# Kernel tuning notes

Measured on AMD Instinct MI355X. Metric: run time of the kernel, lower is better.

## Reference

```python
import jax, jax.numpy as jnp
import numpy as np

IN_SHAPE = (8, 16, 8)     # hidden_shape, prod = 1024
FF_SHAPE = (16, 16, 16)   # ff_shape, prod = 4096
RANKS = (1, 8, 8, 1)      # tt_ranks


def _make_cores(key, in_shape, out_shape, ranks):
    cores = []
    for k in range(3):
        key, sub = jax.random.split(key)
        shape = (ranks[k], in_shape[k], out_shape[k], ranks[k + 1])
        # glorot-ish scale per core
        scale = (2.0 / (in_shape[k] * ranks[k] + out_shape[k] * ranks[k + 1])) ** 0.5
        cores.append(jax.random.normal(sub, shape, dtype=jnp.float32) * scale)
    return key, cores


def setup_inputs() -> dict:
    key = jax.random.key(0)
    key, kx = jax.random.split(key)
    x = jax.random.normal(kx, (8192, int(np.prod(IN_SHAPE))), dtype=jnp.float32)
    key, c0 = _make_cores(key, IN_SHAPE, FF_SHAPE, RANKS)
    key, c1 = _make_cores(key, FF_SHAPE, IN_SHAPE, RANKS)
    b0 = jnp.zeros((int(np.prod(FF_SHAPE)),), dtype=jnp.float32)
    b1 = jnp.zeros((int(np.prod(IN_SHAPE)),), dtype=jnp.float32)
    return {
        "x": x,
        "c0a": c0[0], "c0b": c0[1], "c0c": c0[2], "b0": b0,
        "c1a": c1[0], "c1b": c1[1], "c1c": c1[2], "b1": b1,
    }


def tt_linear(x, cores, bias, in_shape, out_shape):
    # x: (B, prod(in_shape)); cores[k]: (r_k, in_k, out_k, r_{k+1})
    B = x.shape[0]
    t = x.reshape(B, *in_shape)                      # (B, i, j, k)
    t = jnp.einsum('bijk,aior->bjkor', t, cores[0])  # (B, j, k, o1, r1)
    t = jnp.einsum('bjkor,rjps->bkops', t, cores[1]) # (B, k, o1, o2, r2)
    t = jnp.einsum('bkops,skqu->bopq', t, cores[2])  # (B, o1, o2, o3)
    return t.reshape(B, -1) + bias


def reference(x, c0a, c0b, c0c, b0, c1a, c1b, c1c, b1):
    h = tt_linear(x, (c0a, c0b, c0c), b0, IN_SHAPE, FF_SHAPE)
    h = jax.nn.gelu(h, approximate=False)  # nn.GELU default = exact erf form
    out = tt_linear(h, (c1a, c1b, c1c), b1, FF_SHAPE, IN_SHAPE)
    return out
```

## Files before the change

### kernel.cpp

```cpp
#include <hip/hip_runtime.h>
#include <math.h>

typedef _Float16 f16x8 __attribute__((ext_vector_type(8)));
typedef _Float16 f16x4 __attribute__((ext_vector_type(4)));
typedef float f32x16 __attribute__((ext_vector_type(16)));

__device__ __forceinline__ void async_copy16(const void* g, void* l) {
    __builtin_amdgcn_global_load_lds(
        (const __attribute__((address_space(1))) void*)g,
        (__attribute__((address_space(3))) void*)l, 16, 0, 0);
}

__global__ __launch_bounds__(256) void prep_kernel(
    const float* __restrict__ x, _Float16* __restrict__ xh,
    const float* __restrict__ c0a, const float* __restrict__ c0b,
    const float* __restrict__ c0c, _Float16* __restrict__ W0t,
    const float* __restrict__ c1a, const float* __restrict__ c1b,
    const float* __restrict__ c1c, _Float16* __restrict__ W1t) {
    __shared__ float G[16384];
    const int b = blockIdx.x, t = threadIdx.x;
    if (b < 1024) {
        const float4* in4 = (const float4*)x;
        f16x4* out4 = (f16x4*)xh;
        const int base = b * 2048 + t;
#pragma unroll
        for (int u = 0; u < 8; ++u) {
            float4 v = in4[base + u * 256];
            f16x4 o;
            o[0] = (_Float16)v.x; o[1] = (_Float16)v.y;
            o[2] = (_Float16)v.z; o[3] = (_Float16)v.w;
            out4[base + u * 256] = o;
        }
    } else if (b < 1280) {
        const int o = (b - 1024) >> 4, p = (b - 1024) & 15;
        {
            const int h = t >> 7, qk = t & 127, q = qk >> 3, k = qk & 7;
            float cr[8];
#pragma unroll
            for (int ss = 0; ss < 8; ++ss) cr[ss] = c0c[(ss * 8 + k) * 16 + q];
            for (int rj = h * 64; rj < h * 64 + 64; ++rj) {
                const float4* b4 = (const float4*)(c0b + (rj * 16 + p) * 8);
                float4 b0 = b4[0], b1 = b4[1];
                float s = b0.x * cr[0] + b0.y * cr[1] + b0.z * cr[2] + b0.w * cr[3]
                        + b1.x * cr[4] + b1.y * cr[5] + b1.z * cr[6] + b1.w * cr[7];
                G[q * 1024 + rj * 8 + k] = s;
            }
        }
        __syncthreads();
        const int i = t >> 5, j = (t >> 1) & 15, kq = t & 1;
        float a[8];
#pragma unroll
        for (int r = 0; r < 8; ++r) a[r] = c0a[(i * 16 + o) * 8 + r];
        const float4* G4 = (const float4*)G;
#pragma unroll
        for (int q = 0; q < 16; ++q) {
            float4 acc = {0.f, 0.f, 0.f, 0.f};
#pragma unroll
            for (int r = 0; r < 8; ++r) {
                float4 g = G4[q * 256 + r * 32 + j * 2 + kq];
                acc.x += a[r] * g.x; acc.y += a[r] * g.y;
                acc.z += a[r] * g.z; acc.w += a[r] * g.w;
            }
            f16x4 h4;
            h4[0] = (_Float16)acc.x; h4[1] = (_Float16)acc.y;
            h4[2] = (_Float16)acc.z; h4[3] = (_Float16)acc.w;
            *(f16x4*)(W0t + (size_t)((o * 16 + p) * 16 + q) * 1024 + t * 4) = h4;
        }
    } else {
        const int o = (b - 1280) >> 4, p = (b - 1280) & 15;
        {
            const int h = t >> 7, qk = t & 127, q = qk >> 4, k = qk & 15;
            float cr[8];
#pragma unroll
            for (int ss = 0; ss < 8; ++ss) cr[ss] = c1c[(ss * 16 + k) * 8 + q];
            for (int rj = h * 64; rj < h * 64 + 64; ++rj) {
                const float4* b4 = (const float4*)(c1b + (rj * 16 + p) * 8);
                float4 b0 = b4[0], b1 = b4[1];
                float s = b0.x * cr[0] + b0.y * cr[1] + b0.z * cr[2] + b0.w * cr[3]
                        + b1.x * cr[4] + b1.y * cr[5] + b1.z * cr[6] + b1.w * cr[7];
                G[q * 2048 + rj * 16 + k] = s;
            }
        }
        __syncthreads();
        const int ig = t >> 6, j = (t >> 2) & 15, kq = t & 3;
        float a[4][8];
#pragma unroll
        for (int ii = 0; ii < 4; ++ii)
#pragma unroll
            for (int r = 0; r < 8; ++r) a[ii][r] = c1a[((ig * 4 + ii) * 8 + o) * 8 + r];
        const float4* G4 = (const float4*)G;
#pragma unroll
        for (int q = 0; q < 8; ++q) {
            float4 acc[4] = {{0,0,0,0},{0,0,0,0},{0,0,0,0},{0,0,0,0}};
#pragma unroll
            for (int r = 0; r < 8; ++r) {
                float4 g = G4[q * 512 + r * 64 + j * 4 + kq];
#pragma unroll
                for (int ii = 0; ii < 4; ++ii) {
                    acc[ii].x += a[ii][r] * g.x; acc[ii].y += a[ii][r] * g.y;
                    acc[ii].z += a[ii][r] * g.z; acc[ii].w += a[ii][r] * g.w;
                }
            }
            const size_t rowbase = (size_t)((o * 16 + p) * 8 + q) * 4096;
#pragma unroll
            for (int ii = 0; ii < 4; ++ii) {
                f16x4 h4;
                h4[0] = (_Float16)acc[ii].x; h4[1] = (_Float16)acc[ii].y;
                h4[2] = (_Float16)acc[ii].z; h4[3] = (_Float16)acc[ii].w;
                *(f16x4*)(W1t + rowbase + (ig * 4 + ii) * 256 + j * 16 + kq * 4) = h4;
            }
        }
    }
}

template <int OUTMODE>
__global__ __launch_bounds__(256) void gemm32_kernel(
    const _Float16* __restrict__ A, const _Float16* __restrict__ Bt,
    const float* __restrict__ bias, void* __restrict__ Cout,
    int M, int N, int K) {
    constexpr int BK = 64;
    __shared__ alignas(16) _Float16 sA[128 * BK];
    __shared__ alignas(16) _Float16 sB[128 * BK];

    const int t = threadIdx.x, lane = t & 63, w = t >> 6;
    const int m0 = blockIdx.x * 128, n0 = blockIdx.y * 128;
    const int wm = (w & 1) * 64, wn = (w >> 1) * 64;
    const int l31 = lane & 31, lh = lane >> 5;

    f32x16 acc[2][2] = {};

    const int s0 = w * 256 + lane;
    const int row0 = s0 >> 3;
    const int cslot = s0 & 7;
    const int kofs = (cslot ^ (row0 & 7)) * 8;
    const _Float16* gA = A + (size_t)(m0 + row0) * K + kofs;
    const _Float16* gB = Bt + (size_t)(n0 + row0) * K + kofs;
    _Float16* lA = sA + s0 * 8;
    _Float16* lB = sB + s0 * 8;
    const size_t rs = (size_t)8 * K;

    for (int k0 = 0; k0 < K; k0 += BK) {
#pragma unroll
        for (int m = 0; m < 4; ++m) {
            async_copy16(gA + k0 + m * rs, lA + m * 512);
            async_copy16(gB + k0 + m * rs, lB + m * 512);
        }
        __syncthreads();
#pragma unroll
        for (int kk = 0; kk < 4; ++kk) {
            f16x8 af[2], bf[2];
            const int c = kk * 2 + lh;
            const int sl = (c ^ (l31 & 7)) * 8;
#pragma unroll
            for (int i = 0; i < 2; ++i) {
                af[i] = *(const f16x8*)(sA + (wm + i * 32 + l31) * BK + sl);
                bf[i] = *(const f16x8*)(sB + (wn + i * 32 + l31) * BK + sl);
            }
#pragma unroll
            for (int i = 0; i < 2; ++i)
#pragma unroll
                for (int j = 0; j < 2; ++j)
                    acc[i][j] = __builtin_amdgcn_mfma_f32_32x32x16_f16(af[i], bf[j], acc[i][j], 0, 0, 0);
        }
        __syncthreads();
    }

#pragma unroll
    for (int i = 0; i < 2; ++i)
#pragma unroll
        for (int j = 0; j < 2; ++j) {
            const int col = n0 + wn + j * 32 + l31;
            const float bv = bias[col];
            const int rbase = m0 + wm + i * 32 + 4 * lh;
            if (OUTMODE == 1) {
                _Float16* C = (_Float16*)Cout;
#pragma unroll
                for (int r = 0; r < 16; ++r) {
                    int row = rbase + (r & 3) + 8 * (r >> 2);
                    float v = acc[i][j][r] + bv;
                    float uu = v * (0.7978845608028654f + 0.0356774081363001f * v * v);
                    float e = __builtin_amdgcn_exp2f(uu * 2.8853900817779268f);
                    float rc = __builtin_amdgcn_rcpf(e + 1.0f);
                    C[(size_t)row * N + col] = (_Float16)(v * (1.0f - rc));
                }
            } else {
                float* C = (float*)Cout;
#pragma unroll
                for (int r = 0; r < 16; ++r) {
                    int row = rbase + (r & 3) + 8 * (r >> 2);
                    C[(size_t)row * N + col] = acc[i][j][r] + bv;
                }
            }
        }
}

__global__ __launch_bounds__(256) void gemm32_splitk(
    const _Float16* __restrict__ A, const _Float16* __restrict__ Bt,
    float* __restrict__ p0, float* __restrict__ p1,
    int M, int N, int K) {
    constexpr int BK = 64;
    __shared__ alignas(16) _Float16 sA[128 * BK];
    __shared__ alignas(16) _Float16 sB[128 * BK];

    const int t = threadIdx.x, lane = t & 63, w = t >> 6;
    const int m0 = blockIdx.x * 128, n0 = blockIdx.y * 128;
    const int wm = (w & 1) * 64, wn = (w >> 1) * 64;
    const int l31 = lane & 31, lh = lane >> 5;

    f32x16 acc[2][2] = {};

    const int s0 = w * 256 + lane;
    const int row0 = s0 >> 3;
    const int cslot = s0 & 7;
    const int kofs = (cslot ^ (row0 & 7)) * 8;
    const _Float16* gA = A + (size_t)(m0 + row0) * K + kofs;
    const _Float16* gB = Bt + (size_t)(n0 + row0) * K + kofs;
    _Float16* lA = sA + s0 * 8;
    _Float16* lB = sB + s0 * 8;
    const size_t rs = (size_t)8 * K;

    const int kbase = blockIdx.z * (K >> 1);
    const int kend = kbase + (K >> 1);
    for (int k0 = kbase; k0 < kend; k0 += BK) {
#pragma unroll
        for (int m = 0; m < 4; ++m) {
            async_copy16(gA + k0 + m * rs, lA + m * 512);
            async_copy16(gB + k0 + m * rs, lB + m * 512);
        }
        __syncthreads();
#pragma unroll
        for (int kk = 0; kk < 4; ++kk) {
            f16x8 af[2], bf[2];
            const int c = kk * 2 + lh;
            const int sl = (c ^ (l31 & 7)) * 8;
#pragma unroll
            for (int i = 0; i < 2; ++i) {
                af[i] = *(const f16x8*)(sA + (wm + i * 32 + l31) * BK + sl);
                bf[i] = *(const f16x8*)(sB + (wn + i * 32 + l31) * BK + sl);
            }
#pragma unroll
            for (int i = 0; i < 2; ++i)
#pragma unroll
                for (int j = 0; j < 2; ++j)
                    acc[i][j] = __builtin_amdgcn_mfma_f32_32x32x16_f16(af[i], bf[j], acc[i][j], 0, 0, 0);
        }
        __syncthreads();
    }

    float* C = blockIdx.z ? p1 : p0;
#pragma unroll
    for (int i = 0; i < 2; ++i)
#pragma unroll
        for (int j = 0; j < 2; ++j) {
            const int col = n0 + wn + j * 32 + l31;
            const int rbase = m0 + wm + i * 32 + 4 * lh;
#pragma unroll
            for (int r = 0; r < 16; ++r) {
                int row = rbase + (r & 3) + 8 * (r >> 2);
                C[(size_t)row * N + col] = acc[i][j][r];
            }
        }
}

__global__ __launch_bounds__(256) void reduce_bias(
    const float* __restrict__ p1, const float* __restrict__ bias,
    float* __restrict__ out, int total4, int N) {
    const float4* q4 = (const float4*)p1;
    float4* o4 = (float4*)out;
    for (int i = blockIdx.x * 256 + threadIdx.x; i < total4; i += gridDim.x * 256) {
        float4 o = o4[i], q = q4[i];
        const int col = (i << 2) & (N - 1);
        const float4 b = *(const float4*)(bias + col);
        o.x += q.x + b.x; o.y += q.y + b.y;
        o.z += q.z + b.z; o.w += q.w + b.w;
        o4[i] = o;
    }
}

extern "C" void kernel_launch(void* const* d_in, const int* in_sizes, int n_in,
                              void* d_out, int out_size, void* d_ws, size_t ws_size,
                              hipStream_t stream) {
    const float* x   = (const float*)d_in[0];
    const float* c0a = (const float*)d_in[1];
    const float* c0b = (const float*)d_in[2];
    const float* c0c = (const float*)d_in[3];
    const float* b0  = (const float*)d_in[4];
    const float* c1a = (const float*)d_in[5];
    const float* c1b = (const float*)d_in[6];
    const float* c1c = (const float*)d_in[7];
    const float* b1  = (const float*)d_in[8];
    float* out = (float*)d_out;

    char* ws = (char*)d_ws;
    _Float16* xh  = (_Float16*)(ws);
    _Float16* W0t = (_Float16*)(ws + (size_t)(16u << 20));
    _Float16* W1t = (_Float16*)(ws + (size_t)(24u << 20));
    _Float16* h   = (_Float16*)(ws + (size_t)(32u << 20));
    float*    p1  = (float*)   (ws + (size_t)(96u << 20));

    prep_kernel<<<dim3(1408), dim3(256), 0, stream>>>(
        x, xh, c0a, c0b, c0c, W0t, c1a, c1b, c1c, W1t);
    gemm32_kernel<1><<<dim3(64, 32), dim3(256), 0, stream>>>(
        xh, W0t, b0, (void*)h, 8192, 4096, 1024);
    if (ws_size >= ((size_t)128u << 20)) {
        gemm32_splitk<<<dim3(64, 8, 2), dim3(256), 0, stream>>>(
            h, W1t, out, p1, 8192, 1024, 4096);
        reduce_bias<<<dim3(2048), dim3(256), 0, stream>>>(
            p1, b1, out, (8192 * 1024) / 4, 1024);
    } else {
        gemm32_kernel<0><<<dim3(64, 8), dim3(256), 0, stream>>>(
            h, W1t, b1, (void*)out, 8192, 1024, 4096);
    }
}
```

Measured before the change: 283.2 us.

## Replace split-K partial buffer and reduce kernel with atomic adds; split prep blocks

The second GEMM's split-K halves now accumulate directly into the zeroed output with unsafe atomic float adds, with the bias added by the z=0 half. This removes the partial-sum buffer and the separate reduce kernel, at the cost of a memset of the output and atomic traffic. The weight-prep blocks are split in two over q, halving shared memory per block and doubling block count for more parallelism. The fallback path for small workspace is removed.

```diff
diff --git a/kernel.cpp b/kernel.cpp
--- a/kernel.cpp
+++ b/kernel.cpp
@@ -17,7 +17,7 @@
     const float* __restrict__ c0c, _Float16* __restrict__ W0t,
     const float* __restrict__ c1a, const float* __restrict__ c1b,
     const float* __restrict__ c1c, _Float16* __restrict__ W1t) {
-    __shared__ float G[16384];
+    __shared__ float G[8192];
     const int b = blockIdx.x, t = threadIdx.x;
     if (b < 1024) {
         const float4* in4 = (const float4*)x;
@@ -31,19 +31,21 @@
             o[2] = (_Float16)v.z; o[3] = (_Float16)v.w;
             out4[base + u * 256] = o;
         }
-    } else if (b < 1280) {
-        const int o = (b - 1024) >> 4, p = (b - 1024) & 15;
+    } else if (b < 1536) {
+        const int idx = b - 1024;
+        const int o = idx >> 5, p = (idx >> 1) & 15, qh = idx & 1;
         {
-            const int h = t >> 7, qk = t & 127, q = qk >> 3, k = qk & 7;
+            const int h = t >> 6, pair = t & 63, ql = pair >> 3, k = pair & 7;
+            const int q = qh * 8 + ql;
             float cr[8];
 #pragma unroll
             for (int ss = 0; ss < 8; ++ss) cr[ss] = c0c[(ss * 8 + k) * 16 + q];
-            for (int rj = h * 64; rj < h * 64 + 64; ++rj) {
+            for (int rj = h * 32; rj < h * 32 + 32; ++rj) {
                 const float4* b4 = (const float4*)(c0b + (rj * 16 + p) * 8);
                 float4 b0 = b4[0], b1 = b4[1];
                 float s = b0.x * cr[0] + b0.y * cr[1] + b0.z * cr[2] + b0.w * cr[3]
                         + b1.x * cr[4] + b1.y * cr[5] + b1.z * cr[6] + b1.w * cr[7];
-                G[q * 1024 + rj * 8 + k] = s;
+                G[ql * 1024 + rj * 8 + k] = s;
             }
         }
         __syncthreads();
@@ -53,11 +55,12 @@
         for (int r = 0; r < 8; ++r) a[r] = c0a[(i * 16 + o) * 8 + r];
         const float4* G4 = (const float4*)G;
 #pragma unroll
-        for (int q = 0; q < 16; ++q) {
+        for (int ql = 0; ql < 8; ++ql) {
+            const int q = qh * 8 + ql;
             float4 acc = {0.f, 0.f, 0.f, 0.f};
 #pragma unroll
             for (int r = 0; r < 8; ++r) {
-                float4 g = G4[q * 256 + r * 32 + j * 2 + kq];
+                float4 g = G4[ql * 256 + r * 32 + j * 2 + kq];
                 acc.x += a[r] * g.x; acc.y += a[r] * g.y;
                 acc.z += a[r] * g.z; acc.w += a[r] * g.w;
             }
@@ -67,18 +70,20 @@
             *(f16x4*)(W0t + (size_t)((o * 16 + p) * 16 + q) * 1024 + t * 4) = h4;
         }
     } else {
-        const int o = (b - 1280) >> 4, p = (b - 1280) & 15;
+        const int idx = b - 1536;
+        const int o = idx >> 5, p = (idx >> 1) & 15, qh = idx & 1;
         {
-            const int h = t >> 7, qk = t & 127, q = qk >> 4, k = qk & 15;
+            const int h = t >> 6, pair = t & 63, ql = pair >> 4, k = pair & 15;
+            const int q = qh * 4 + ql;
             float cr[8];
 #pragma unroll
             for (int ss = 0; ss < 8; ++ss) cr[ss] = c1c[(ss * 16 + k) * 8 + q];
-            for (int rj = h * 64; rj < h * 64 + 64; ++rj) {
+            for (int rj = h * 32; rj < h * 32 + 32; ++rj) {
                 const float4* b4 = (const float4*)(c1b + (rj * 16 + p) * 8);
                 float4 b0 = b4[0], b1 = b4[1];
                 float s = b0.x * cr[0] + b0.y * cr[1] + b0.z * cr[2] + b0.w * cr[3]
                         + b1.x * cr[4] + b1.y * cr[5] + b1.z * cr[6] + b1.w * cr[7];
-                G[q * 2048 + rj * 16 + k] = s;
+                G[ql * 2048 + rj * 16 + k] = s;
             }
         }
         __syncthreads();
@@ -90,11 +95,12 @@
             for (int r = 0; r < 8; ++r) a[ii][r] = c1a[((ig * 4 + ii) * 8 + o) * 8 + r];
         const float4* G4 = (const float4*)G;
 #pragma unroll
-        for (int q = 0; q < 8; ++q) {
+        for (int ql = 0; ql < 4; ++ql) {
+            const int q = qh * 4 + ql;
             float4 acc[4] = {{0,0,0,0},{0,0,0,0},{0,0,0,0},{0,0,0,0}};
 #pragma unroll
             for (int r = 0; r < 8; ++r) {
-                float4 g = G4[q * 512 + r * 64 + j * 4 + kq];
+                float4 g = G4[ql * 512 + r * 64 + j * 4 + kq];
 #pragma unroll
                 for (int ii = 0; ii < 4; ++ii) {
                     acc[ii].x += a[ii][r] * g.x; acc[ii].y += a[ii][r] * g.y;
@@ -194,9 +200,9 @@
         }
 }
 
-__global__ __launch_bounds__(256) void gemm32_splitk(
+__global__ __launch_bounds__(256) void gemm32_splitk_atomic(
     const _Float16* __restrict__ A, const _Float16* __restrict__ Bt,
-    float* __restrict__ p0, float* __restrict__ p1,
+    const float* __restrict__ bias, float* __restrict__ out,
     int M, int N, int K) {
     constexpr int BK = 64;
     __shared__ alignas(16) _Float16 sA[128 * BK];
@@ -247,34 +253,19 @@
         __syncthreads();
     }
 
-    float* C = blockIdx.z ? p1 : p0;
 #pragma unroll
     for (int i = 0; i < 2; ++i)
 #pragma unroll
         for (int j = 0; j < 2; ++j) {
             const int col = n0 + wn + j * 32 + l31;
+            const float bv = (blockIdx.z == 0) ? bias[col] : 0.f;
             const int rbase = m0 + wm + i * 32 + 4 * lh;
 #pragma unroll
             for (int r = 0; r < 16; ++r) {
                 int row = rbase + (r & 3) + 8 * (r >> 2);
-                C[(size_t)row * N + col] = acc[i][j][r];
-            }
-        }
-}
-
-__global__ __launch_bounds__(256) void reduce_bias(
-    const float* __restrict__ p1, const float* __restrict__ bias,
-    float* __restrict__ out, int total4, int N) {
-    const float4* q4 = (const float4*)p1;
-    float4* o4 = (float4*)out;
-    for (int i = blockIdx.x * 256 + threadIdx.x; i < total4; i += gridDim.x * 256) {
-        float4 o = o4[i], q = q4[i];
-        const int col = (i << 2) & (N - 1);
-        const float4 b = *(const float4*)(bias + col);
-        o.x += q.x + b.x; o.y += q.y + b.y;
-        o.z += q.z + b.z; o.w += q.w + b.w;
-        o4[i] = o;
-    }
+                unsafeAtomicAdd(&out[(size_t)row * N + col], acc[i][j][r] + bv);
+            }
+        }
 }
 
 extern "C" void kernel_launch(void* const* d_in, const int* in_sizes, int n_in,
@@ -296,19 +287,12 @@
     _Float16* W0t = (_Float16*)(ws + (size_t)(16u << 20));
     _Float16* W1t = (_Float16*)(ws + (size_t)(24u << 20));
     _Float16* h   = (_Float16*)(ws + (size_t)(32u << 20));
-    float*    p1  = (float*)   (ws + (size_t)(96u << 20));
-
-    prep_kernel<<<dim3(1408), dim3(256), 0, stream>>>(
+
+    hipMemsetAsync(out, 0, (size_t)8192 * 1024 * sizeof(float), stream);
+    prep_kernel<<<dim3(1792), dim3(256), 0, stream>>>(
         x, xh, c0a, c0b, c0c, W0t, c1a, c1b, c1c, W1t);
     gemm32_kernel<1><<<dim3(64, 32), dim3(256), 0, stream>>>(
         xh, W0t, b0, (void*)h, 8192, 4096, 1024);
-    if (ws_size >= ((size_t)128u << 20)) {
-        gemm32_splitk<<<dim3(64, 8, 2), dim3(256), 0, stream>>>(
-            h, W1t, out, p1, 8192, 1024, 4096);
-        reduce_bias<<<dim3(2048), dim3(256), 0, stream>>>(
-            p1, b1, out, (8192 * 1024) / 4, 1024);
-    } else {
-        gemm32_kernel<0><<<dim3(64, 8), dim3(256), 0, stream>>>(
-            h, W1t, b1, (void*)out, 8192, 1024, 4096);
-    }
-}
+    gemm32_splitk_atomic<<<dim3(64, 8, 2), dim3(256), 0, stream>>>(
+        h, W1t, b1, out, 8192, 1024, 4096);
+}
```

Result: slower. 314.5 us (+11.1%).

## Fuse split-K reduction into one 512-thread block via LDS exchange

Applied to the files above, without the earlier changes.

The second GEMM's split-K now runs both K halves as two 256-thread groups inside a single 512-thread block. The second group's partial accumulators are combined with the first group's through shared memory, and bias is added before one write. This removes the fp32 partial buffer round-trip to global memory and the separate reduce_bias launch. The prep kernel is also split into separate cast and weight-build kernels. The cost is 64KB of LDS per block and larger blocks, which lowers occupancy, and the __syncthreads calls now stall both groups together.

```diff
diff --git a/kernel.cpp b/kernel.cpp
--- a/kernel.cpp
+++ b/kernel.cpp
@@ -11,28 +11,30 @@
         (__attribute__((address_space(3))) void*)l, 16, 0, 0);
 }
 
-__global__ __launch_bounds__(256) void prep_kernel(
-    const float* __restrict__ x, _Float16* __restrict__ xh,
+__global__ __launch_bounds__(256) void cast_kernel(
+    const float* __restrict__ x, _Float16* __restrict__ xh) {
+    const float4* in4 = (const float4*)x;
+    f16x4* out4 = (f16x4*)xh;
+    const int base = blockIdx.x * 2048 + threadIdx.x;
+#pragma unroll
+    for (int u = 0; u < 8; ++u) {
+        float4 v = in4[base + u * 256];
+        f16x4 o;
+        o[0] = (_Float16)v.x; o[1] = (_Float16)v.y;
+        o[2] = (_Float16)v.z; o[3] = (_Float16)v.w;
+        out4[base + u * 256] = o;
+    }
+}
+
+__global__ __launch_bounds__(256) void weight_kernel(
     const float* __restrict__ c0a, const float* __restrict__ c0b,
     const float* __restrict__ c0c, _Float16* __restrict__ W0t,
     const float* __restrict__ c1a, const float* __restrict__ c1b,
     const float* __restrict__ c1c, _Float16* __restrict__ W1t) {
     __shared__ float G[16384];
     const int b = blockIdx.x, t = threadIdx.x;
-    if (b < 1024) {
-        const float4* in4 = (const float4*)x;
-        f16x4* out4 = (f16x4*)xh;
-        const int base = b * 2048 + t;
-#pragma unroll
-        for (int u = 0; u < 8; ++u) {
-            float4 v = in4[base + u * 256];
-            f16x4 o;
-            o[0] = (_Float16)v.x; o[1] = (_Float16)v.y;
-            o[2] = (_Float16)v.z; o[3] = (_Float16)v.w;
-            out4[base + u * 256] = o;
-        }
-    } else if (b < 1280) {
-        const int o = (b - 1024) >> 4, p = (b - 1024) & 15;
+    if (b < 256) {
+        const int o = b >> 4, p = b & 15;
         {
             const int h = t >> 7, qk = t & 127, q = qk >> 3, k = qk & 7;
             float cr[8];
@@ -67,7 +69,8 @@
             *(f16x4*)(W0t + (size_t)((o * 16 + p) * 16 + q) * 1024 + t * 4) = h4;
         }
     } else {
-        const int o = (b - 1280) >> 4, p = (b - 1280) & 15;
+        const int idx = b - 256;
+        const int o = idx >> 4, p = idx & 15;
         {
             const int h = t >> 7, qk = t & 127, q = qk >> 4, k = qk & 15;
             float cr[8];
@@ -194,22 +197,26 @@
         }
 }
 
-__global__ __launch_bounds__(256) void gemm32_splitk(
+__global__ __launch_bounds__(512) void gemm32_splitk_lds(
     const _Float16* __restrict__ A, const _Float16* __restrict__ Bt,
-    float* __restrict__ p0, float* __restrict__ p1,
+    const float* __restrict__ bias, float* __restrict__ out,
     int M, int N, int K) {
     constexpr int BK = 64;
-    __shared__ alignas(16) _Float16 sA[128 * BK];
-    __shared__ alignas(16) _Float16 sB[128 * BK];
-
-    const int t = threadIdx.x, lane = t & 63, w = t >> 6;
+    __shared__ alignas(16) _Float16 smem[32768];
+
+    const int t = threadIdx.x;
+    const int g = t >> 8, tl = t & 255;
+    const int lane = tl & 63, wg = tl >> 6;
     const int m0 = blockIdx.x * 128, n0 = blockIdx.y * 128;
-    const int wm = (w & 1) * 64, wn = (w >> 1) * 64;
+    const int wm = (wg & 1) * 64, wn = (wg >> 1) * 64;
     const int l31 = lane & 31, lh = lane >> 5;
 
+    _Float16* sA = smem + g * 16384;
+    _Float16* sB = sA + 8192;
+
     f32x16 acc[2][2] = {};
 
-    const int s0 = w * 256 + lane;
+    const int s0 = wg * 256 + lane;
     const int row0 = s0 >> 3;
     const int cslot = s0 & 7;
     const int kofs = (cslot ^ (row0 & 7)) * 8;
@@ -219,7 +226,7 @@
     _Float16* lB = sB + s0 * 8;
     const size_t rs = (size_t)8 * K;
 
-    const int kbase = blockIdx.z * (K >> 1);
+    const int kbase = g * (K >> 1);
     const int kend = kbase + (K >> 1);
     for (int k0 = kbase; k0 < kend; k0 += BK) {
 #pragma unroll
@@ -247,33 +254,32 @@
         __syncthreads();
     }
 
-    float* C = blockIdx.z ? p1 : p0;
-#pragma unroll
-    for (int i = 0; i < 2; ++i)
-#pragma unroll
-        for (int j = 0; j < 2; ++j) {
-            const int col = n0 + wn + j * 32 + l31;
-            const int rbase = m0 + wm + i * 32 + 4 * lh;
-#pragma unroll
-            for (int r = 0; r < 16; ++r) {
-                int row = rbase + (r & 3) + 8 * (r >> 2);
-                C[(size_t)row * N + col] = acc[i][j][r];
-            }
-        }
-}
-
-__global__ __launch_bounds__(256) void reduce_bias(
-    const float* __restrict__ p1, const float* __restrict__ bias,
-    float* __restrict__ out, int total4, int N) {
-    const float4* q4 = (const float4*)p1;
-    float4* o4 = (float4*)out;
-    for (int i = blockIdx.x * 256 + threadIdx.x; i < total4; i += gridDim.x * 256) {
-        float4 o = o4[i], q = q4[i];
-        const int col = (i << 2) & (N - 1);
-        const float4 b = *(const float4*)(bias + col);
-        o.x += q.x + b.x; o.y += q.y + b.y;
-        o.z += q.z + b.z; o.w += q.w + b.w;
-        o4[i] = o;
+    float* xch = (float*)smem;
+    if (g == 1) {
+#pragma unroll
+        for (int i = 0; i < 2; ++i)
+#pragma unroll
+            for (int j = 0; j < 2; ++j)
+#pragma unroll
+                for (int r = 0; r < 16; ++r)
+                    xch[((i * 2 + j) * 16 + r) * 256 + tl] = acc[i][j][r];
+    }
+    __syncthreads();
+    if (g == 0) {
+#pragma unroll
+        for (int i = 0; i < 2; ++i)
+#pragma unroll
+            for (int j = 0; j < 2; ++j) {
+                const int col = n0 + wn + j * 32 + l31;
+                const float bv = bias[col];
+                const int rbase = m0 + wm + i * 32 + 4 * lh;
+#pragma unroll
+                for (int r = 0; r < 16; ++r) {
+                    int row = rbase + (r & 3) + 8 * (r >> 2);
+                    float v = acc[i][j][r] + xch[((i * 2 + j) * 16 + r) * 256 + tl] + bv;
+                    out[(size_t)row * N + col] = v;
+                }
+            }
     }
 }
 
@@ -296,19 +302,12 @@
     _Float16* W0t = (_Float16*)(ws + (size_t)(16u << 20));
     _Float16* W1t = (_Float16*)(ws + (size_t)(24u << 20));
     _Float16* h   = (_Float16*)(ws + (size_t)(32u << 20));
-    float*    p1  = (float*)   (ws + (size_t)(96u << 20));
-
-    prep_kernel<<<dim3(1408), dim3(256), 0, stream>>>(
-        x, xh, c0a, c0b, c0c, W0t, c1a, c1b, c1c, W1t);
+
+    cast_kernel<<<dim3(1024), dim3(256), 0, stream>>>(x, xh);
+    weight_kernel<<<dim3(384), dim3(256), 0, stream>>>(
+        c0a, c0b, c0c, W0t, c1a, c1b, c1c, W1t);
     gemm32_kernel<1><<<dim3(64, 32), dim3(256), 0, stream>>>(
         xh, W0t, b0, (void*)h, 8192, 4096, 1024);
-    if (ws_size >= ((size_t)128u << 20)) {
-        gemm32_splitk<<<dim3(64, 8, 2), dim3(256), 0, stream>>>(
-            h, W1t, out, p1, 8192, 1024, 4096);
-        reduce_bias<<<dim3(2048), dim3(256), 0, stream>>>(
-            p1, b1, out, (8192 * 1024) / 4, 1024);
-    } else {
-        gemm32_kernel<0><<<dim3(64, 8), dim3(256), 0, stream>>>(
-            h, W1t, b1, (void*)out, 8192, 1024, 4096);
-    }
-}
+    gemm32_splitk_lds<<<dim3(64, 8), dim3(512), 0, stream>>>(
+        h, W1t, b1, out, 8192, 1024, 4096);
+}
```

Result: faster. 265.7 us (-6.2%).
